# Performance work log

Measured on AMD Instinct MI355X. Metric: run time of the kernel, lower is better.

## Reference

```python
import jax, jax.numpy as jnp
import numpy as np

N = 100000   # graph nodes
E = 600000   # edges
D = 128      # feature_dim
K = 3        # candidate ops per MixedOp
EPS = 1e-5   # BatchNorm eps


def _param_stack(key, n_ops):
    kW, kb = jax.random.split(key)
    W = jax.random.normal(kW, (n_ops, K, D, D), jnp.float32) * (1.0 / np.sqrt(D))
    b = jax.random.normal(kb, (n_ops, K, D), jnp.float32) * 0.01
    g = jnp.ones((n_ops, K, D), jnp.float32)
    be = jnp.zeros((n_ops, K, D), jnp.float32)
    return W, b, g, be


def setup_inputs() -> dict:
    key = jax.random.key(0)
    ks = jax.random.split(key, 16)
    inp = {
        'src_emb': jax.random.normal(ks[0], (N, D), jnp.float32),
        'hr': jax.random.normal(ks[1], (N, D), jnp.float32),
        'edge_src': jax.random.randint(ks[2], (E,), 0, N),
        'edge_dst': jax.random.randint(ks[3], (E,), 0, N),
        'weights_zero': jax.random.uniform(ks[4], (1, K), jnp.float32),
        'weights_first': jax.random.uniform(ks[5], (3, K), jnp.float32),
        'weights_middle': jax.random.uniform(ks[6], (2, K), jnp.float32),
        'weights_last': jax.random.uniform(ks[7], (2, K), jnp.float32),
    }
    for name, k, n_ops in [('zero', ks[8], 1), ('first', ks[9], 3), ('mid', ks[10], 2), ('last', ks[11], 2)]:
        W, b, g, be = _param_stack(k, n_ops)
        inp[f'W_{name}'] = W; inp[f'b_{name}'] = b
        inp[f'g_{name}'] = g; inp[f'be_{name}'] = be
    inp['W_cat'] = jax.random.normal(ks[12], (3 * D, D), jnp.float32) * (1.0 / np.sqrt(3 * D))
    inp['b_cat'] = jax.random.normal(ks[13], (D,), jnp.float32) * 0.01
    inp['g_cat'] = jnp.ones((D,), jnp.float32)
    inp['be_cat'] = jnp.zeros((D,), jnp.float32)
    return inp


def _mean_agg(h, src, dst):
    s = jax.ops.segment_sum(h[src], dst, num_segments=N)            # [N,D]
    deg = jax.ops.segment_sum(jnp.ones((src.shape[0],), h.dtype), dst, num_segments=N)
    return s / jnp.maximum(deg, 1.0)[:, None]


def _max_agg(h, src, dst):
    m = jax.ops.segment_max(h[src], dst, num_segments=N)            # -inf for empty segs
    return jnp.where(jnp.isfinite(m), m, 0.0)


def _mixed(cands, w, W, b, g, be):
    # cands: list of K [N,D]; w:[K]; W:[K,D,D]; b/g/be:[K,D]
    x = jnp.stack(cands)                                            # [K,N,D]
    y = jnp.einsum('knd,kdf->knf', x, W) + b[:, None, :]            # Linear per candidate
    mu = jnp.mean(y, axis=1, keepdims=True)                         # BatchNorm1d (batch stats)
    var = jnp.var(y, axis=1, keepdims=True)
    y = (y - mu) * jax.lax.rsqrt(var + EPS) * g[:, None, :] + be[:, None, :]
    y = jax.nn.relu(y)
    return jnp.einsum('k,knd->nd', w, y)                            # alpha-weighted sum


def _graph_cands(h, src, dst):
    return [h, _mean_agg(h, src, dst), _max_agg(h, src, dst)]


def _cell_forward(src_emb, hr, edge_src, edge_dst,
                  weights_zero, weights_first, weights_middle, weights_last,
                  W_zero, b_zero, g_zero, be_zero,
                  W_first, b_first, g_first, be_first,
                  W_mid, b_mid, g_mid, be_mid,
                  W_last, b_last, g_last, be_last,
                  W_cat, b_cat, g_cat, be_cat):
    src, dst = edge_src, edge_dst
    # Cell_Zero: relation-composition candidates on (src_emb, hr)
    pre = [src_emb, src_emb - hr, src_emb * hr]
    h_in = _mixed(pre, weights_zero[0], W_zero[0], b_zero[0], g_zero[0], be_zero[0])
    # Cell_First (nodes=2): ops layout [(i=0,j=0),(i=1,j=0),(i=1,j=1)]
    states = [h_in]
    s0 = _mixed(_graph_cands(states[0], src, dst), weights_first[0], W_first[0], b_first[0], g_first[0], be_first[0])
    states.append(s0)
    s1 = (_mixed(_graph_cands(states[0], src, dst), weights_first[1], W_first[1], b_first[1], g_first[1], be_first[1])
          + _mixed(_graph_cands(states[1], src, dst), weights_first[2], W_first[2], b_first[2], g_first[2], be_first[2]))
    states.append(s1)
    states = states[1:]                                             # drop h_in -> len 2
    # Cell_Middle (nodes=2): one MixedOp per state
    states = [_mixed(_graph_cands(states[i], src, dst), weights_middle[i], W_mid[i], b_mid[i], g_mid[i], be_mid[i])
              for i in range(2)]
    # Cell_Last (in_nodes=2, nodes=1): one new state from both inputs; returns all 3
    s_last = (_mixed(_graph_cands(states[0], src, dst), weights_last[0], W_last[0], b_last[0], g_last[0], be_last[0])
              + _mixed(_graph_cands(states[1], src, dst), weights_last[1], W_last[1], b_last[1], g_last[1], be_last[1]))
    states = states + [s_last]                                      # len 3
    # concat -> Linear -> BN -> ReLU (dropout p=0)
    h = jnp.concatenate(states, axis=1) @ W_cat + b_cat             # [N,D]
    mu = jnp.mean(h, axis=0, keepdims=True)
    var = jnp.var(h, axis=0, keepdims=True)
    h = (h - mu) * jax.lax.rsqrt(var + EPS) * g_cat + be_cat
    return jax.nn.relu(h)


def reference(src_emb, hr, edge_src, edge_dst,
              weights_zero, weights_first, weights_middle, weights_last,
              W_zero, b_zero, g_zero, be_zero,
              W_first, b_first, g_first, be_first,
              W_mid, b_mid, g_mid, be_mid,
              W_last, b_last, g_last, be_last,
              W_cat, b_cat, g_cat, be_cat):
    return _cell_forward(src_emb, hr, edge_src, edge_dst,
                         weights_zero, weights_first, weights_middle, weights_last,
                         W_zero, b_zero, g_zero, be_zero,
                         W_first, b_first, g_first, be_first,
                         W_mid, b_mid, g_mid, be_mid,
                         W_last, b_last, g_last, be_last,
                         W_cat, b_cat, g_cat, be_cat)
```

## Files before the change

### kernel.cpp

```cpp
#include <hip/hip_runtime.h>

#define N_NODES 100000
#define N_EDGES 600000
#define NPAD    100096
#define NTILES  782
#define SCAN_B  98
#define EPS_F   1e-5f

typedef __bf16 bf16_t;
typedef __bf16 bf16x8 __attribute__((ext_vector_type(8)));
typedef __bf16 bf16x4 __attribute__((ext_vector_type(4)));
typedef float  f32x4  __attribute__((ext_vector_type(4)));

__global__ __launch_bounds__(256)
void init_zero_kernel(int* __restrict__ deg, float* __restrict__ stats)
{
    int i = blockIdx.x * 256 + threadIdx.x;
    if (i < N_NODES) deg[i] = 0;
    if (i < 9 * 768) stats[i] = 0.f;
}

__global__ __launch_bounds__(256)
void transpose_w_kernel(const float* __restrict__ Wz, const float* __restrict__ Wf,
                        const float* __restrict__ Wm, const float* __restrict__ Wl,
                        const float* __restrict__ Wc, bf16_t* __restrict__ wt)
{
    int idx = blockIdx.x * 256 + threadIdx.x;
    int mat = idx >> 14;
    int off = idx & 16383;
    int n = off >> 7, kk = off & 127;
    const float* src;
    if      (mat < 3)  src = Wz + mat * 16384;
    else if (mat < 12) src = Wf + (mat - 3) * 16384;
    else if (mat < 18) src = Wm + (mat - 12) * 16384;
    else if (mat < 24) src = Wl + (mat - 18) * 16384;
    else               src = Wc + (mat - 24) * 16384;
    wt[idx] = (bf16_t)src[kk * 128 + n];
}

__global__ __launch_bounds__(256)
void pre_kernel(const float* __restrict__ se, const float* __restrict__ hr,
                bf16_t* __restrict__ p0, bf16_t* __restrict__ p1, bf16_t* __restrict__ p2)
{
    long i = ((long)blockIdx.x * 256 + threadIdx.x) * 8;
    float4 a0 = *(const float4*)&se[i], a1 = *(const float4*)&se[i + 4];
    float4 b0 = *(const float4*)&hr[i], b1 = *(const float4*)&hr[i + 4];
    float av[8] = {a0.x, a0.y, a0.z, a0.w, a1.x, a1.y, a1.z, a1.w};
    float bv[8] = {b0.x, b0.y, b0.z, b0.w, b1.x, b1.y, b1.z, b1.w};
    bf16x8 o0, o1, o2;
#pragma unroll
    for (int j = 0; j < 8; ++j) {
        o0[j] = (bf16_t)av[j];
        o1[j] = (bf16_t)(av[j] - bv[j]);
        o2[j] = (bf16_t)(av[j] * bv[j]);
    }
    *(bf16x8*)&p0[i] = o0;
    *(bf16x8*)&p1[i] = o1;
    *(bf16x8*)&p2[i] = o2;
}

__global__ __launch_bounds__(256)
void deg_count_kernel(const int* __restrict__ dst, int* __restrict__ deg)
{
    int i = blockIdx.x * 256 + threadIdx.x;
    if (i < N_EDGES) atomicAdd(&deg[dst[i]], 1);
}

__global__ __launch_bounds__(256)
void scan_a_kernel(const int* __restrict__ deg, int* __restrict__ partials)
{
    __shared__ int ls[256];
    int b = blockIdx.x, t = threadIdx.x;
    int s = 0;
    for (int j = 0; j < 4; ++j) {
        int i = b * 1024 + t * 4 + j;
        if (i < N_NODES) s += deg[i];
    }
    ls[t] = s; __syncthreads();
    for (int o = 128; o > 0; o >>= 1) {
        if (t < o) ls[t] += ls[t + o];
        __syncthreads();
    }
    if (t == 0) partials[b] = ls[0];
}

__global__ void scan_b_kernel(const int* __restrict__ partials, int* __restrict__ pofs)
{
    if (threadIdx.x == 0) {
        int a = 0;
        for (int i = 0; i < SCAN_B; ++i) { pofs[i] = a; a += partials[i]; }
    }
}

__global__ __launch_bounds__(256)
void scan_c_kernel(const int* __restrict__ deg, const int* __restrict__ pofs,
                   int* __restrict__ row_ptr, int* __restrict__ cursor)
{
    __shared__ int ls[256];
    int b = blockIdx.x, t = threadIdx.x;
    int v[4], s = 0;
    for (int j = 0; j < 4; ++j) {
        int i = b * 1024 + t * 4 + j;
        v[j] = (i < N_NODES) ? deg[i] : 0;
        s += v[j];
    }
    ls[t] = s; __syncthreads();
    for (int o = 1; o < 256; o <<= 1) {
        int tv = (t >= o) ? ls[t - o] : 0;
        __syncthreads();
        ls[t] += tv;
        __syncthreads();
    }
    int excl = ls[t] - s + pofs[b];
    for (int j = 0; j < 4; ++j) {
        int i = b * 1024 + t * 4 + j;
        if (i < N_NODES) { row_ptr[i] = excl; cursor[i] = excl; excl += v[j]; }
    }
    if (b == 0 && t == 0) row_ptr[N_NODES] = N_EDGES;
}

__global__ __launch_bounds__(256)
void scatter_kernel(const int* __restrict__ src, const int* __restrict__ dst,
                    int* __restrict__ cursor, int* __restrict__ csr_src)
{
    int i = blockIdx.x * 256 + threadIdx.x;
    if (i < N_EDGES) {
        int p = atomicAdd(&cursor[dst[i]], 1);
        csr_src[p] = src[i];
    }
}

__global__ __launch_bounds__(256)
void agg_kernel(const bf16_t* __restrict__ h, const int* __restrict__ row_ptr,
                const int* __restrict__ csr_src,
                bf16_t* __restrict__ mean_o, bf16_t* __restrict__ max_o)
{
    int node = blockIdx.x * 16 + (threadIdx.x >> 4);
    int dd = (threadIdx.x & 15) * 8;
    int e0 = row_ptr[node], e1 = row_ptr[node + 1];
    float s[8], mx[8];
#pragma unroll
    for (int j = 0; j < 8; ++j) { s[j] = 0.f; mx[j] = 0.f; }
    for (int e = e0; e < e1; ++e) {
        int sc = csr_src[e];
        bf16x8 v = *(const bf16x8*)&h[(long)sc * 128 + dd];
#pragma unroll
        for (int j = 0; j < 8; ++j) {
            float f = (float)v[j];
            s[j] += f;
            mx[j] = fmaxf(mx[j], f);
        }
    }
    float inv = 1.f / fmaxf((float)(e1 - e0), 1.f);
    bf16x8 om, ox;
#pragma unroll
    for (int j = 0; j < 8; ++j) { om[j] = (bf16_t)(s[j] * inv); ox[j] = (bf16_t)mx[j]; }
    *(bf16x8*)&mean_o[(long)node * 128 + dd] = om;
    *(bf16x8*)&max_o [(long)node * 128 + dd] = ox;
}

__global__ __launch_bounds__(256, 2)
void gemm_kernel(const bf16_t* __restrict__ x0, const bf16_t* __restrict__ x1,
                 const bf16_t* __restrict__ x2, const bf16_t* __restrict__ wt,
                 const float* __restrict__ bias, bf16_t* __restrict__ out,
                 float* __restrict__ partial, int mode)
{
    __shared__ bf16_t lds_w[16384];
    __shared__ bf16_t lds_x[16384];
    const int tid  = threadIdx.x;
    const int lane = tid & 63;
    const int wave = tid >> 6;
    const int quad = lane >> 4;
    const int t16  = lane & 15;
    const int wr = wave >> 1, wc = wave & 1;
    const long tile_base = (long)blockIdx.x * 128;

    f32x4 acc[4][4];
#pragma unroll
    for (int a = 0; a < 4; ++a)
#pragma unroll
        for (int b = 0; b < 4; ++b) acc[a][b] = (f32x4){0.f, 0.f, 0.f, 0.f};

    const int k_sel = blockIdx.y;
    const int nchunk = (mode == 0) ? 1 : 3;
    const bf16_t* xk = (k_sel == 0) ? x0 : ((k_sel == 1) ? x1 : x2);
    bf16_t* outp = (mode == 0) ? (out + (long)k_sel * NPAD * 128) : out;
    const float* bp = (mode == 0) ? (bias + k_sel * 128) : bias;

    for (int c3 = 0; c3 < nchunk; ++c3) {
        const bf16_t* xcur = (mode == 0) ? xk : ((c3 == 0) ? x0 : ((c3 == 1) ? x1 : x2));
        const bf16_t* wcur = (mode == 0) ? (wt + k_sel * 16384) : (wt + c3 * 16384);
        if (c3) __syncthreads();
#pragma unroll
        for (int i = 0; i < 8; ++i) {
            int idx = tid + i * 256;
            int row = idx >> 4, c = idx & 15;
            int sw = c ^ (row & 15);
            *(uint4*)&lds_w[row * 128 + sw * 8] = *(const uint4*)&wcur[row * 128 + c * 8];
            *(uint4*)&lds_x[row * 128 + sw * 8] = *(const uint4*)&xcur[(tile_base + row) * 128 + c * 8];
        }
        __syncthreads();
#pragma unroll
        for (int ks = 0; ks < 4; ++ks) {
            bf16x8 xf[4], wf[4];
#pragma unroll
            for (int ms = 0; ms < 4; ++ms) {
                int row = wr * 64 + ms * 16 + t16;
                int sw = (ks * 4 + quad) ^ t16;
                xf[ms] = *(const bf16x8*)&lds_x[row * 128 + sw * 8];
            }
#pragma unroll
            for (int ns = 0; ns < 4; ++ns) {
                int row = wc * 64 + ns * 16 + t16;
                int sw = (ks * 4 + quad) ^ t16;
                wf[ns] = *(const bf16x8*)&lds_w[row * 128 + sw * 8];
            }
#pragma unroll
            for (int ns = 0; ns < 4; ++ns)
#pragma unroll
                for (int ms = 0; ms < 4; ++ms)
                    acc[ns][ms] = __builtin_amdgcn_mfma_f32_16x16x32_bf16(
                        wf[ns], xf[ms], acc[ns][ms], 0, 0, 0);
        }
    }

    float ss[16], sq[16];
#pragma unroll
    for (int i = 0; i < 16; ++i) { ss[i] = 0.f; sq[i] = 0.f; }

#pragma unroll
    for (int ms = 0; ms < 4; ++ms) {
        long m = tile_base + wr * 64 + ms * 16 + t16;
        if (m < N_NODES) {
#pragma unroll
            for (int ns = 0; ns < 4; ++ns) {
                int n0 = wc * 64 + ns * 16 + quad * 4;
                float4 b4 = *(const float4*)&bp[n0];
                float v0 = acc[ns][ms][0] + b4.x;
                float v1 = acc[ns][ms][1] + b4.y;
                float v2 = acc[ns][ms][2] + b4.z;
                float v3 = acc[ns][ms][3] + b4.w;
                ss[ns * 4 + 0] += v0; sq[ns * 4 + 0] += v0 * v0;
                ss[ns * 4 + 1] += v1; sq[ns * 4 + 1] += v1 * v1;
                ss[ns * 4 + 2] += v2; sq[ns * 4 + 2] += v2 * v2;
                ss[ns * 4 + 3] += v3; sq[ns * 4 + 3] += v3 * v3;
                bf16x4 ov;
                ov[0] = (bf16_t)v0; ov[1] = (bf16_t)v1;
                ov[2] = (bf16_t)v2; ov[3] = (bf16_t)v3;
                *(bf16x4*)&outp[m * 128 + n0] = ov;
            }
        }
    }

#pragma unroll
    for (int o = 1; o < 16; o <<= 1) {
#pragma unroll
        for (int i = 0; i < 16; ++i) {
            ss[i] += __shfl_xor(ss[i], o);
            sq[i] += __shfl_xor(sq[i], o);
        }
    }

    __syncthreads();
    float* lred = (float*)lds_w;
    if (t16 == 0) {
#pragma unroll
        for (int i = 0; i < 16; ++i) {
            lred[wave * 128 + quad * 32 + i]      = ss[i];
            lred[wave * 128 + quad * 32 + 16 + i] = sq[i];
        }
    }
    __syncthreads();
    {
        int t = tid;
        int d   = t & 127;
        int sel = (t >> 7) * 16;
        int dwc = d >> 6;
        int q   = (d >> 2) & 3;
        int i   = ((d >> 4) & 3) * 4 + (d & 3);
        float v = lred[(0 * 2 + dwc) * 128 + q * 32 + sel + i]
                + lred[(1 * 2 + dwc) * 128 + q * 32 + sel + i];
        long pidx = ((long)((mode == 0) ? k_sel : 0) * NTILES + blockIdx.x) * 256 + t;
        partial[pidx] = v;
    }
}

__global__ __launch_bounds__(256)
void reduce_stats_kernel(const float* __restrict__ partial, float* __restrict__ st)
{
    int k = blockIdx.x, j = blockIdx.y, t = threadIdx.x;
    int b0 = j * 98, b1 = (b0 + 98 < NTILES) ? b0 + 98 : NTILES;
    float s = 0.f;
    const float* p = partial + (long)k * NTILES * 256 + t;
    for (int b = b0; b < b1; ++b) s += p[(long)b * 256];
    atomicAdd(&st[k * 256 + t], s);
}

__global__ __launch_bounds__(256)
void passc_kernel(const bf16_t* __restrict__ y, const float* __restrict__ st,
                  const float* __restrict__ g, const float* __restrict__ be,
                  const float* __restrict__ w, bf16_t* __restrict__ out, int accflag)
{
    long base = ((long)blockIdx.x * 256 + threadIdx.x) * 8;
    int d0 = (int)(base & 127);
    const float invN = 1.0f / (float)N_NODES;
    float res[8];
    if (accflag) {
        bf16x8 pv = *(const bf16x8*)&out[base];
#pragma unroll
        for (int j = 0; j < 8; ++j) res[j] = (float)pv[j];
    } else {
#pragma unroll
        for (int j = 0; j < 8; ++j) res[j] = 0.f;
    }
#pragma unroll
    for (int k = 0; k < 3; ++k) {
        bf16x8 yv = *(const bf16x8*)&y[(long)k * NPAD * 128 + base];
        float wk = w[k];
#pragma unroll
        for (int j = 0; j < 8; ++j) {
            int d = d0 + j;
            float mu  = st[k * 256 + d] * invN;
            float var = st[k * 256 + 128 + d] * invN - mu * mu;
            float rs  = rsqrtf(var + EPS_F);
            float v = ((float)yv[j] - mu) * rs * g[k * 128 + d] + be[k * 128 + d];
            res[j] += wk * fmaxf(v, 0.f);
        }
    }
    bf16x8 ov;
#pragma unroll
    for (int j = 0; j < 8; ++j) ov[j] = (bf16_t)res[j];
    *(bf16x8*)&out[base] = ov;
}

__global__ __launch_bounds__(256)
void final_kernel(const bf16_t* __restrict__ h, const float* __restrict__ st,
                  const float* __restrict__ g, const float* __restrict__ be,
                  float* __restrict__ out)
{
    long base = ((long)blockIdx.x * 256 + threadIdx.x) * 8;
    int d0 = (int)(base & 127);
    const float invN = 1.0f / (float)N_NODES;
    bf16x8 hv = *(const bf16x8*)&h[base];
    float ov[8];
#pragma unroll
    for (int j = 0; j < 8; ++j) {
        int d = d0 + j;
        float mu  = st[d] * invN;
        float var = st[128 + d] * invN - mu * mu;
        float rs  = rsqrtf(var + EPS_F);
        float v = ((float)hv[j] - mu) * rs * g[d] + be[d];
        ov[j] = fmaxf(v, 0.f);
    }
    *(float4*)&out[base]     = (float4){ov[0], ov[1], ov[2], ov[3]};
    *(float4*)&out[base + 4] = (float4){ov[4], ov[5], ov[6], ov[7]};
}

extern "C" void kernel_launch(void* const* d_in, const int* in_sizes, int n_in,
                              void* d_out, int out_size, void* d_ws, size_t ws_size,
                              hipStream_t stream)
{
    const float* src_emb = (const float*)d_in[0];
    const float* hr      = (const float*)d_in[1];
    const int*   e_src   = (const int*)d_in[2];
    const int*   e_dst   = (const int*)d_in[3];
    const float* w_zero  = (const float*)d_in[4];
    const float* w_first = (const float*)d_in[5];
    const float* w_mid   = (const float*)d_in[6];
    const float* w_last  = (const float*)d_in[7];
    const float* W_zero  = (const float*)d_in[8];
    const float* b_zero  = (const float*)d_in[9];
    const float* g_zero  = (const float*)d_in[10];
    const float* be_zero = (const float*)d_in[11];
    const float* W_first = (const float*)d_in[12];
    const float* b_first = (const float*)d_in[13];
    const float* g_first = (const float*)d_in[14];
    const float* be_first= (const float*)d_in[15];
    const float* W_mid   = (const float*)d_in[16];
    const float* b_mid   = (const float*)d_in[17];
    const float* g_mid   = (const float*)d_in[18];
    const float* be_mid  = (const float*)d_in[19];
    const float* W_last  = (const float*)d_in[20];
    const float* b_last  = (const float*)d_in[21];
    const float* g_last  = (const float*)d_in[22];
    const float* be_last = (const float*)d_in[23];
    const float* W_cat   = (const float*)d_in[24];
    const float* b_cat   = (const float*)d_in[25];
    const float* g_cat   = (const float*)d_in[26];
    const float* be_cat  = (const float*)d_in[27];
    float* out = (float*)d_out;

    char* ws = (char*)d_ws;
    size_t off = 0;
    auto carve = [&](size_t bytes) -> char* {
        off = (off + 255) & ~(size_t)255;
        char* p = ws + off;
        off += bytes;
        return p;
    };

    const size_t SB = (size_t)NPAD * 128 * sizeof(bf16_t);
    bf16_t* B[8];
    for (int i = 0; i < 8; ++i) B[i] = (bf16_t*)carve(SB);
    bf16_t* ybuf = B[0];
    bf16_t* wt    = (bf16_t*)carve((size_t)27 * 16384 * 2);
    float*  stats = (float*)carve(9 * 768 * sizeof(float));
    float*  partial = (float*)carve((size_t)3 * NTILES * 256 * sizeof(float));
    int* deg    = (int*)carve((size_t)N_NODES * 4);
    int* rowp   = (int*)carve((size_t)(N_NODES + 1) * 4);
    int* cursor = (int*)carve((size_t)N_NODES * 4);
    int* csr    = (int*)carve((size_t)N_EDGES * 4);
    int* parts  = (int*)carve(SCAN_B * 4);
    int* pofs   = (int*)carve(SCAN_B * 4);

    bf16_t* wtZ  = wt;
    bf16_t* wtF0 = wt + (size_t)3  * 16384;
    bf16_t* wtF1 = wt + (size_t)6  * 16384;
    bf16_t* wtF2 = wt + (size_t)9  * 16384;
    bf16_t* wtM0 = wt + (size_t)12 * 16384;
    bf16_t* wtM1 = wt + (size_t)15 * 16384;
    bf16_t* wtL0 = wt + (size_t)18 * 16384;
    bf16_t* wtL1 = wt + (size_t)21 * 16384;
    bf16_t* wtC  = wt + (size_t)24 * 16384;

    float* st0 = stats + 0 * 768;
    float* st1 = stats + 1 * 768;
    float* st2 = stats + 2 * 768;
    float* st3 = stats + 3 * 768;
    float* st4 = stats + 4 * 768;
    float* st5 = stats + 5 * 768;
    float* st6 = stats + 6 * 768;
    float* st7 = stats + 7 * 768;
    float* st8 = stats + 8 * 768;

    const int GEL8 = (N_NODES * 128) / 2048;

    init_zero_kernel<<<dim3((N_NODES + 255) / 256), dim3(256), 0, stream>>>(deg, stats);
    transpose_w_kernel<<<dim3(1728), dim3(256), 0, stream>>>(W_zero, W_first, W_mid, W_last, W_cat, wt);
    deg_count_kernel<<<dim3((N_EDGES + 255) / 256), dim3(256), 0, stream>>>(e_dst, deg);
    scan_a_kernel<<<dim3(SCAN_B), dim3(256), 0, stream>>>(deg, parts);
    scan_b_kernel<<<dim3(1), dim3(64), 0, stream>>>(parts, pofs);
    scan_c_kernel<<<dim3(SCAN_B), dim3(256), 0, stream>>>(deg, pofs, rowp, cursor);
    scatter_kernel<<<dim3((N_EDGES + 255) / 256), dim3(256), 0, stream>>>(e_src, e_dst, cursor, csr);

    auto G = [&](const bf16_t* x0_, const bf16_t* x1_, const bf16_t* x2_,
                 const bf16_t* w_, const float* b_, bf16_t* o_, float* st_, int mode) {
        int nk = (mode == 0) ? 3 : 1;
        gemm_kernel<<<dim3(NTILES, nk), dim3(256), 0, stream>>>(
            x0_, x1_, x2_, w_, b_, o_, partial, mode);
        reduce_stats_kernel<<<dim3(nk, 8), dim3(256), 0, stream>>>(partial, st_);
    };
    auto C = [&](const float* g_, const float* be_, const float* w_, float* st_,
                 bf16_t* o_, int acc) {
        passc_kernel<<<dim3(GEL8), dim3(256), 0, stream>>>(ybuf, st_, g_, be_, w_, o_, acc);
    };
    auto A = [&](const bf16_t* h_, bf16_t* me_, bf16_t* mx_) {
        agg_kernel<<<dim3(N_NODES / 16), dim3(256), 0, stream>>>(h_, rowp, csr, me_, mx_);
    };

    pre_kernel<<<dim3(GEL8), dim3(256), 0, stream>>>(src_emb, hr, B[3], B[4], B[5]);
    G(B[3], B[4], B[5], wtZ, b_zero, ybuf, st0, 0);
    C(g_zero, be_zero, w_zero, st0, B[6], 0);

    A(B[6], B[3], B[4]);

    G(B[6], B[3], B[4], wtF0, b_first + 0 * 384, ybuf, st1, 0);
    C(g_first + 0 * 384, be_first + 0 * 384, w_first + 0, st1, B[5], 0);

    G(B[6], B[3], B[4], wtF1, b_first + 1 * 384, ybuf, st2, 0);
    C(g_first + 1 * 384, be_first + 1 * 384, w_first + 3, st2, B[7], 0);

    A(B[5], B[3], B[4]);

    G(B[5], B[3], B[4], wtF2, b_first + 2 * 384, ybuf, st3, 0);
    C(g_first + 2 * 384, be_first + 2 * 384, w_first + 6, st3, B[7], 1);

    G(B[5], B[3], B[4], wtM0, b_mid + 0 * 384, ybuf, st4, 0);
    C(g_mid + 0 * 384, be_mid + 0 * 384, w_mid + 0, st4, B[6], 0);

    A(B[7], B[3], B[4]);

    G(B[7], B[3], B[4], wtM1, b_mid + 1 * 384, ybuf, st5, 0);
    C(g_mid + 1 * 384, be_mid + 1 * 384, w_mid + 3, st5, B[5], 0);

    A(B[6], B[3], B[4]);
    G(B[6], B[3], B[4], wtL0, b_last + 0 * 384, ybuf, st6, 0);
    C(g_last + 0 * 384, be_last + 0 * 384, w_last + 0, st6, B[7], 0);
    A(B[5], B[3], B[4]);
    G(B[5], B[3], B[4], wtL1, b_last + 1 * 384, ybuf, st7, 0);
    C(g_last + 1 * 384, be_last + 1 * 384, w_last + 3, st7, B[7], 1);

    G(B[6], B[5], B[7], wtC, b_cat, B[0], st8, 1);
    final_kernel<<<dim3(GEL8), dim3(256), 0, stream>>>(B[0], st8, g_cat, be_cat, out);
}
```

Measured before the change: 1.247 ms.

## Load GEMM MFMA fragments directly from global memory, drop LDS staging

New measurement: 1.350 ms. 1.08x slower.

```diff
diff --git a/kernel.cpp b/kernel.cpp
--- a/kernel.cpp
+++ b/kernel.cpp
@@ -159,14 +159,13 @@
     *(bf16x8*)&max_o [(long)node * 128 + dd] = ox;
 }
 
-__global__ __launch_bounds__(256, 2)
+__global__ __launch_bounds__(256, 3)
 void gemm_kernel(const bf16_t* __restrict__ x0, const bf16_t* __restrict__ x1,
                  const bf16_t* __restrict__ x2, const bf16_t* __restrict__ wt,
                  const float* __restrict__ bias, bf16_t* __restrict__ out,
                  float* __restrict__ partial, int mode)
 {
-    __shared__ bf16_t lds_w[16384];
-    __shared__ bf16_t lds_x[16384];
+    __shared__ float lred[512];
     const int tid  = threadIdx.x;
     const int lane = tid & 63;
     const int wave = tid >> 6;
@@ -190,31 +189,18 @@
     for (int c3 = 0; c3 < nchunk; ++c3) {
         const bf16_t* xcur = (mode == 0) ? xk : ((c3 == 0) ? x0 : ((c3 == 1) ? x1 : x2));
         const bf16_t* wcur = (mode == 0) ? (wt + k_sel * 16384) : (wt + c3 * 16384);
-        if (c3) __syncthreads();
-#pragma unroll
-        for (int i = 0; i < 8; ++i) {
-            int idx = tid + i * 256;
-            int row = idx >> 4, c = idx & 15;
-            int sw = c ^ (row & 15);
-            *(uint4*)&lds_w[row * 128 + sw * 8] = *(const uint4*)&wcur[row * 128 + c * 8];
-            *(uint4*)&lds_x[row * 128 + sw * 8] = *(const uint4*)&xcur[(tile_base + row) * 128 + c * 8];
-        }
-        __syncthreads();
+        const bf16_t* wlane = wcur + (wc * 64 + t16) * 128 + quad * 8;
+        const bf16_t* xlane = xcur + (tile_base + wr * 64 + t16) * 128 + quad * 8;
 #pragma unroll
         for (int ks = 0; ks < 4; ++ks) {
-            bf16x8 xf[4], wf[4];
-#pragma unroll
-            for (int ms = 0; ms < 4; ++ms) {
-                int row = wr * 64 + ms * 16 + t16;
-                int sw = (ks * 4 + quad) ^ t16;
-                xf[ms] = *(const bf16x8*)&lds_x[row * 128 + sw * 8];
-            }
-#pragma unroll
-            for (int ns = 0; ns < 4; ++ns) {
-                int row = wc * 64 + ns * 16 + t16;
-                int sw = (ks * 4 + quad) ^ t16;
-                wf[ns] = *(const bf16x8*)&lds_w[row * 128 + sw * 8];
-            }
+            bf16x8 wf[4];
+#pragma unroll
+            for (int ns = 0; ns < 4; ++ns)
+                wf[ns] = *(const bf16x8*)&wlane[ns * 16 * 128 + ks * 32];
+            bf16x8 xf[4];
+#pragma unroll
+            for (int ms = 0; ms < 4; ++ms)
+                xf[ms] = *(const bf16x8*)&xlane[ms * 16 * 128 + ks * 32];
 #pragma unroll
             for (int ns = 0; ns < 4; ++ns)
 #pragma unroll
@@ -261,8 +247,6 @@
         }
     }
 
-    __syncthreads();
-    float* lred = (float*)lds_w;
     if (t16 == 0) {
 #pragma unroll
         for (int i = 0; i < 16; ++i) {
```

## Recompute GEMMs instead of storing pre-BN outputs; fuse BN-apply into second GEMM pass

Applied to the files above, without the earlier changes.

After: 1.270 ms. Within noise of the previous version (+1.8%).

```diff
diff --git a/kernel.cpp b/kernel.cpp
--- a/kernel.cpp
+++ b/kernel.cpp
@@ -160,10 +160,10 @@
 }
 
 __global__ __launch_bounds__(256, 2)
-void gemm_kernel(const bf16_t* __restrict__ x0, const bf16_t* __restrict__ x1,
-                 const bf16_t* __restrict__ x2, const bf16_t* __restrict__ wt,
-                 const float* __restrict__ bias, bf16_t* __restrict__ out,
-                 float* __restrict__ partial, int mode)
+void gemm_stats_kernel(const bf16_t* __restrict__ x0, const bf16_t* __restrict__ x1,
+                       const bf16_t* __restrict__ x2, const bf16_t* __restrict__ wt,
+                       const float* __restrict__ bias,
+                       float* __restrict__ partial, int mode)
 {
     __shared__ bf16_t lds_w[16384];
     __shared__ bf16_t lds_x[16384];
@@ -184,7 +184,6 @@
     const int k_sel = blockIdx.y;
     const int nchunk = (mode == 0) ? 1 : 3;
     const bf16_t* xk = (k_sel == 0) ? x0 : ((k_sel == 1) ? x1 : x2);
-    bf16_t* outp = (mode == 0) ? (out + (long)k_sel * NPAD * 128) : out;
     const float* bp = (mode == 0) ? (bias + k_sel * 128) : bias;
 
     for (int c3 = 0; c3 < nchunk; ++c3) {
@@ -244,10 +243,6 @@
                 ss[ns * 4 + 1] += v1; sq[ns * 4 + 1] += v1 * v1;
                 ss[ns * 4 + 2] += v2; sq[ns * 4 + 2] += v2 * v2;
                 ss[ns * 4 + 3] += v3; sq[ns * 4 + 3] += v3 * v3;
-                bf16x4 ov;
-                ov[0] = (bf16_t)v0; ov[1] = (bf16_t)v1;
-                ov[2] = (bf16_t)v2; ov[3] = (bf16_t)v3;
-                *(bf16x4*)&outp[m * 128 + n0] = ov;
             }
         }
     }
@@ -296,64 +291,191 @@
     atomicAdd(&st[k * 256 + t], s);
 }
 
-__global__ __launch_bounds__(256)
-void passc_kernel(const bf16_t* __restrict__ y, const float* __restrict__ st,
-                  const float* __restrict__ g, const float* __restrict__ be,
-                  const float* __restrict__ w, bf16_t* __restrict__ out, int accflag)
-{
-    long base = ((long)blockIdx.x * 256 + threadIdx.x) * 8;
-    int d0 = (int)(base & 127);
+__global__ __launch_bounds__(256, 2)
+void gemm_apply_kernel(const bf16_t* __restrict__ x0, const bf16_t* __restrict__ x1,
+                       const bf16_t* __restrict__ x2, const bf16_t* __restrict__ wt,
+                       const float* __restrict__ bias, const float* __restrict__ st,
+                       const float* __restrict__ g, const float* __restrict__ be,
+                       const float* __restrict__ wvec,
+                       bf16_t* __restrict__ outb, float* __restrict__ outf,
+                       int accflag, int mode)
+{
+    __shared__ bf16_t lds_w[16384];
+    __shared__ bf16_t lds_x[16384];
+    const int tid  = threadIdx.x;
+    const int lane = tid & 63;
+    const int wave = tid >> 6;
+    const int quad = lane >> 4;
+    const int t16  = lane & 15;
+    const int wr = wave >> 1, wc = wave & 1;
+    const long tile_base = (long)blockIdx.x * 128;
     const float invN = 1.0f / (float)N_NODES;
-    float res[8];
-    if (accflag) {
-        bf16x8 pv = *(const bf16x8*)&out[base];
-#pragma unroll
-        for (int j = 0; j < 8; ++j) res[j] = (float)pv[j];
+
+    f32x4 res[4][4];
+    if (mode == 0 && accflag) {
+#pragma unroll
+        for (int ms = 0; ms < 4; ++ms) {
+            long m = tile_base + wr * 64 + ms * 16 + t16;
+            bool ok = (m < N_NODES);
+#pragma unroll
+            for (int ns = 0; ns < 4; ++ns) {
+                int n0 = wc * 64 + ns * 16 + quad * 4;
+                if (ok) {
+                    bf16x4 pv = *(const bf16x4*)&outb[m * 128 + n0];
+                    res[ns][ms] = (f32x4){(float)pv[0], (float)pv[1], (float)pv[2], (float)pv[3]};
+                } else {
+                    res[ns][ms] = (f32x4){0.f, 0.f, 0.f, 0.f};
+                }
+            }
+        }
     } else {
 #pragma unroll
-        for (int j = 0; j < 8; ++j) res[j] = 0.f;
-    }
-#pragma unroll
+        for (int a = 0; a < 4; ++a)
+#pragma unroll
+            for (int b = 0; b < 4; ++b) res[a][b] = (f32x4){0.f, 0.f, 0.f, 0.f};
+    }
+
+    f32x4 acc[4][4];
+#pragma unroll
+    for (int a = 0; a < 4; ++a)
+#pragma unroll
+        for (int b = 0; b < 4; ++b) acc[a][b] = (f32x4){0.f, 0.f, 0.f, 0.f};
+
     for (int k = 0; k < 3; ++k) {
-        bf16x8 yv = *(const bf16x8*)&y[(long)k * NPAD * 128 + base];
-        float wk = w[k];
-#pragma unroll
-        for (int j = 0; j < 8; ++j) {
-            int d = d0 + j;
-            float mu  = st[k * 256 + d] * invN;
-            float var = st[k * 256 + 128 + d] * invN - mu * mu;
-            float rs  = rsqrtf(var + EPS_F);
-            float v = ((float)yv[j] - mu) * rs * g[k * 128 + d] + be[k * 128 + d];
-            res[j] += wk * fmaxf(v, 0.f);
-        }
-    }
-    bf16x8 ov;
-#pragma unroll
-    for (int j = 0; j < 8; ++j) ov[j] = (bf16_t)res[j];
-    *(bf16x8*)&out[base] = ov;
-}
-
-__global__ __launch_bounds__(256)
-void final_kernel(const bf16_t* __restrict__ h, const float* __restrict__ st,
-                  const float* __restrict__ g, const float* __restrict__ be,
-                  float* __restrict__ out)
-{
-    long base = ((long)blockIdx.x * 256 + threadIdx.x) * 8;
-    int d0 = (int)(base & 127);
-    const float invN = 1.0f / (float)N_NODES;
-    bf16x8 hv = *(const bf16x8*)&h[base];
-    float ov[8];
-#pragma unroll
-    for (int j = 0; j < 8; ++j) {
-        int d = d0 + j;
-        float mu  = st[d] * invN;
-        float var = st[128 + d] * invN - mu * mu;
-        float rs  = rsqrtf(var + EPS_F);
-        float v = ((float)hv[j] - mu) * rs * g[d] + be[d];
-        ov[j] = fmaxf(v, 0.f);
-    }
-    *(float4*)&out[base]     = (float4){ov[0], ov[1], ov[2], ov[3]};
-    *(float4*)&out[base + 4] = (float4){ov[4], ov[5], ov[6], ov[7]};
+        const bf16_t* xcur = (k == 0) ? x0 : ((k == 1) ? x1 : x2);
+        const bf16_t* wcur = wt + k * 16384;
+        if (k) __syncthreads();
+#pragma unroll
+        for (int i = 0; i < 8; ++i) {
+            int idx = tid + i * 256;
+            int row = idx >> 4, c = idx & 15;
+            int sw = c ^ (row & 15);
+            *(uint4*)&lds_w[row * 128 + sw * 8] = *(const uint4*)&wcur[row * 128 + c * 8];
+            *(uint4*)&lds_x[row * 128 + sw * 8] = *(const uint4*)&xcur[(tile_base + row) * 128 + c * 8];
+        }
+        __syncthreads();
+
+        if (mode == 0) {
+#pragma unroll
+            for (int a = 0; a < 4; ++a)
+#pragma unroll
+                for (int b = 0; b < 4; ++b) acc[a][b] = (f32x4){0.f, 0.f, 0.f, 0.f};
+        }
+
+#pragma unroll
+        for (int ks = 0; ks < 4; ++ks) {
+            bf16x8 xf[4], wf[4];
+#pragma unroll
+            for (int ms = 0; ms < 4; ++ms) {
+                int row = wr * 64 + ms * 16 + t16;
+                int sw = (ks * 4 + quad) ^ t16;
+                xf[ms] = *(const bf16x8*)&lds_x[row * 128 + sw * 8];
+            }
+#pragma unroll
+            for (int ns = 0; ns < 4; ++ns) {
+                int row = wc * 64 + ns * 16 + t16;
+                int sw = (ks * 4 + quad) ^ t16;
+                wf[ns] = *(const bf16x8*)&lds_w[row * 128 + sw * 8];
+            }
+#pragma unroll
+            for (int ns = 0; ns < 4; ++ns)
+#pragma unroll
+                for (int ms = 0; ms < 4; ++ms)
+                    acc[ns][ms] = __builtin_amdgcn_mfma_f32_16x16x32_bf16(
+                        wf[ns], xf[ms], acc[ns][ms], 0, 0, 0);
+        }
+
+        if (mode == 0) {
+            float wk = wvec[k];
+#pragma unroll
+            for (int ns = 0; ns < 4; ++ns) {
+                int n0 = wc * 64 + ns * 16 + quad * 4;
+                float4 sv = *(const float4*)&st[k * 256 + n0];
+                float4 qv = *(const float4*)&st[k * 256 + 128 + n0];
+                float4 gv = *(const float4*)&g[k * 128 + n0];
+                float4 ev = *(const float4*)&be[k * 128 + n0];
+                float4 bv = *(const float4*)&bias[k * 128 + n0];
+                float svx[4] = {sv.x, sv.y, sv.z, sv.w};
+                float qvx[4] = {qv.x, qv.y, qv.z, qv.w};
+                float gvx[4] = {gv.x, gv.y, gv.z, gv.w};
+                float evx[4] = {ev.x, ev.y, ev.z, ev.w};
+                float bvx[4] = {bv.x, bv.y, bv.z, bv.w};
+                f32x4 A, C;
+#pragma unroll
+                for (int j = 0; j < 4; ++j) {
+                    float mu  = svx[j] * invN;
+                    float var = qvx[j] * invN - mu * mu;
+                    float rs  = rsqrtf(var + EPS_F);
+                    A[j] = rs * gvx[j];
+                    C[j] = (bvx[j] - mu) * A[j] + evx[j];
+                }
+#pragma unroll
+                for (int ms = 0; ms < 4; ++ms)
+#pragma unroll
+                    for (int j = 0; j < 4; ++j)
+                        res[ns][ms][j] += wk * fmaxf(acc[ns][ms][j] * A[j] + C[j], 0.f);
+            }
+        }
+    }
+
+    if (mode == 0) {
+#pragma unroll
+        for (int ms = 0; ms < 4; ++ms) {
+            long m = tile_base + wr * 64 + ms * 16 + t16;
+            if (m < N_NODES) {
+#pragma unroll
+                for (int ns = 0; ns < 4; ++ns) {
+                    int n0 = wc * 64 + ns * 16 + quad * 4;
+                    bf16x4 ov;
+                    ov[0] = (bf16_t)res[ns][ms][0];
+                    ov[1] = (bf16_t)res[ns][ms][1];
+                    ov[2] = (bf16_t)res[ns][ms][2];
+                    ov[3] = (bf16_t)res[ns][ms][3];
+                    *(bf16x4*)&outb[m * 128 + n0] = ov;
+                }
+            }
+        }
+    } else {
+        f32x4 A4[4], C4[4];
+#pragma unroll
+        for (int ns = 0; ns < 4; ++ns) {
+            int n0 = wc * 64 + ns * 16 + quad * 4;
+            float4 sv = *(const float4*)&st[n0];
+            float4 qv = *(const float4*)&st[128 + n0];
+            float4 gv = *(const float4*)&g[n0];
+            float4 ev = *(const float4*)&be[n0];
+            float4 bv = *(const float4*)&bias[n0];
+            float svx[4] = {sv.x, sv.y, sv.z, sv.w};
+            float qvx[4] = {qv.x, qv.y, qv.z, qv.w};
+            float gvx[4] = {gv.x, gv.y, gv.z, gv.w};
+            float evx[4] = {ev.x, ev.y, ev.z, ev.w};
+            float bvx[4] = {bv.x, bv.y, bv.z, bv.w};
+#pragma unroll
+            for (int j = 0; j < 4; ++j) {
+                float mu  = svx[j] * invN;
+                float var = qvx[j] * invN - mu * mu;
+                float rs  = rsqrtf(var + EPS_F);
+                A4[ns][j] = rs * gvx[j];
+                C4[ns][j] = (bvx[j] - mu) * A4[ns][j] + evx[j];
+            }
+        }
+#pragma unroll
+        for (int ms = 0; ms < 4; ++ms) {
+            long m = tile_base + wr * 64 + ms * 16 + t16;
+            if (m < N_NODES) {
+#pragma unroll
+                for (int ns = 0; ns < 4; ++ns) {
+                    int n0 = wc * 64 + ns * 16 + quad * 4;
+                    float4 o;
+                    o.x = fmaxf(acc[ns][ms][0] * A4[ns][0] + C4[ns][0], 0.f);
+                    o.y = fmaxf(acc[ns][ms][1] * A4[ns][1] + C4[ns][1], 0.f);
+                    o.z = fmaxf(acc[ns][ms][2] * A4[ns][2] + C4[ns][2], 0.f);
+                    o.w = fmaxf(acc[ns][ms][3] * A4[ns][3] + C4[ns][3], 0.f);
+                    *(float4*)&outf[m * 128 + n0] = o;
+                }
+            }
+        }
+    }
 }
 
 extern "C" void kernel_launch(void* const* d_in, const int* in_sizes, int n_in,
@@ -400,9 +522,8 @@
     };
 
     const size_t SB = (size_t)NPAD * 128 * sizeof(bf16_t);
-    bf16_t* B[8];
-    for (int i = 0; i < 8; ++i) B[i] = (bf16_t*)carve(SB);
-    bf16_t* ybuf = B[0];
+    bf16_t* B[6];
+    for (int i = 0; i < 6; ++i) B[i] = (bf16_t*)carve(SB);
     bf16_t* wt    = (bf16_t*)carve((size_t)27 * 16384 * 2);
     float*  stats = (float*)carve(9 * 768 * sizeof(float));
     float*  partial = (float*)carve((size_t)3 * NTILES * 256 * sizeof(float));
@@ -443,53 +564,65 @@
     scan_c_kernel<<<dim3(SCAN_B), dim3(256), 0, stream>>>(deg, pofs, rowp, cursor);
     scatter_kernel<<<dim3((N_EDGES + 255) / 256), dim3(256), 0, stream>>>(e_src, e_dst, cursor, csr);
 
-    auto G = [&](const bf16_t* x0_, const bf16_t* x1_, const bf16_t* x2_,
-                 const bf16_t* w_, const float* b_, bf16_t* o_, float* st_, int mode) {
+    auto S = [&](const bf16_t* x0_, const bf16_t* x1_, const bf16_t* x2_,
+                 const bf16_t* w_, const float* b_, float* st_, int mode) {
         int nk = (mode == 0) ? 3 : 1;
-        gemm_kernel<<<dim3(NTILES, nk), dim3(256), 0, stream>>>(
-            x0_, x1_, x2_, w_, b_, o_, partial, mode);
+        gemm_stats_kernel<<<dim3(NTILES, nk), dim3(256), 0, stream>>>(
+            x0_, x1_, x2_, w_, b_, partial, mode);
         reduce_stats_kernel<<<dim3(nk, 8), dim3(256), 0, stream>>>(partial, st_);
     };
-    auto C = [&](const float* g_, const float* be_, const float* w_, float* st_,
+    auto P = [&](const bf16_t* x0_, const bf16_t* x1_, const bf16_t* x2_,
+                 const bf16_t* w_, const float* b_, float* st_,
+                 const float* g_, const float* be_, const float* wv_,
                  bf16_t* o_, int acc) {
-        passc_kernel<<<dim3(GEL8), dim3(256), 0, stream>>>(ybuf, st_, g_, be_, w_, o_, acc);
+        gemm_apply_kernel<<<dim3(NTILES), dim3(256), 0, stream>>>(
+            x0_, x1_, x2_, w_, b_, st_, g_, be_, wv_, o_, nullptr, acc, 0);
     };
     auto A = [&](const bf16_t* h_, bf16_t* me_, bf16_t* mx_) {
         agg_kernel<<<dim3(N_NODES / 16), dim3(256), 0, stream>>>(h_, rowp, csr, me_, mx_);
     };
 
-    pre_kernel<<<dim3(GEL8), dim3(256), 0, stream>>>(src_emb, hr, B[3], B[4], B[5]);
-    G(B[3], B[4], B[5], wtZ, b_zero, ybuf, st0, 0);
-    C(g_zero, be_zero, w_zero, st0, B[6], 0);
-
-    A(B[6], B[3], B[4]);
-
-    G(B[6], B[3], B[4], wtF0, b_first + 0 * 384, ybuf, st1, 0);
-    C(g_first + 0 * 384, be_first + 0 * 384, w_first + 0, st1, B[5], 0);
-
-    G(B[6], B[3], B[4], wtF1, b_first + 1 * 384, ybuf, st2, 0);
-    C(g_first + 1 * 384, be_first + 1 * 384, w_first + 3, st2, B[7], 0);
-
-    A(B[5], B[3], B[4]);
-
-    G(B[5], B[3], B[4], wtF2, b_first + 2 * 384, ybuf, st3, 0);
-    C(g_first + 2 * 384, be_first + 2 * 384, w_first + 6, st3, B[7], 1);
-
-    G(B[5], B[3], B[4], wtM0, b_mid + 0 * 384, ybuf, st4, 0);
-    C(g_mid + 0 * 384, be_mid + 0 * 384, w_mid + 0, st4, B[6], 0);
-
-    A(B[7], B[3], B[4]);
-
-    G(B[7], B[3], B[4], wtM1, b_mid + 1 * 384, ybuf, st5, 0);
-    C(g_mid + 1 * 384, be_mid + 1 * 384, w_mid + 3, st5, B[5], 0);
-
-    A(B[6], B[3], B[4]);
-    G(B[6], B[3], B[4], wtL0, b_last + 0 * 384, ybuf, st6, 0);
-    C(g_last + 0 * 384, be_last + 0 * 384, w_last + 0, st6, B[7], 0);
-    A(B[5], B[3], B[4]);
-    G(B[5], B[3], B[4], wtL1, b_last + 1 * 384, ybuf, st7, 0);
-    C(g_last + 1 * 384, be_last + 1 * 384, w_last + 3, st7, B[7], 1);
-
-    G(B[6], B[5], B[7], wtC, b_cat, B[0], st8, 1);
-    final_kernel<<<dim3(GEL8), dim3(256), 0, stream>>>(B[0], st8, g_cat, be_cat, out);
-}
+    pre_kernel<<<dim3(GEL8), dim3(256), 0, stream>>>(src_emb, hr, B[0], B[1], B[2]);
+    S(B[0], B[1], B[2], wtZ, b_zero, st0, 0);
+    P(B[0], B[1], B[2], wtZ, b_zero, st0, g_zero, be_zero, w_zero, B[3], 0);
+
+    A(B[3], B[4], B[5]);
+
+    S(B[3], B[4], B[5], wtF0, b_first + 0 * 384, st1, 0);
+    P(B[3], B[4], B[5], wtF0, b_first + 0 * 384, st1,
+      g_first + 0 * 384, be_first + 0 * 384, w_first + 0, B[0], 0);
+
+    S(B[3], B[4], B[5], wtF1, b_first + 1 * 384, st2, 0);
+    P(B[3], B[4], B[5], wtF1, b_first + 1 * 384, st2,
+      g_first + 1 * 384, be_first + 1 * 384, w_first + 3, B[1], 0);
+
+    A(B[0], B[2], B[3]);
+
+    S(B[0], B[2], B[3], wtF2, b_first + 2 * 384, st3, 0);
+    P(B[0], B[2], B[3], wtF2, b_first + 2 * 384, st3,
+      g_first + 2 * 384, be_first + 2 * 384, w_first + 6, B[1], 1);
+
+    S(B[0], B[2], B[3], wtM0, b_mid + 0 * 384, st4, 0);
+    P(B[0], B[2], B[3], wtM0, b_mid + 0 * 384, st4,
+      g_mid + 0 * 384, be_mid + 0 * 384, w_mid + 0, B[4], 0);
+
+    A(B[1], B[0], B[2]);
+
+    S(B[1], B[0], B[2], wtM1, b_mid + 1 * 384, st5, 0);
+    P(B[1], B[0], B[2], wtM1, b_mid + 1 * 384, st5,
+      g_mid + 1 * 384, be_mid + 1 * 384, w_mid + 3, B[5], 0);
+
+    A(B[4], B[0], B[1]);
+    S(B[4], B[0], B[1], wtL0, b_last + 0 * 384, st6, 0);
+    P(B[4], B[0], B[1], wtL0, b_last + 0 * 384, st6,
+      g_last + 0 * 384, be_last + 0 * 384, w_last + 0, B[2], 0);
+    A(B[5], B[0], B[1]);
+    S(B[5], B[0], B[1], wtL1, b_last + 1 * 384, st7, 0);
+    P(B[5], B[0], B[1], wtL1, b_last + 1 * 384, st7,
+      g_last + 1 * 384, be_last + 1 * 384, w_last + 3, B[2], 1);
+
+    S(B[4], B[5], B[2], wtC, b_cat, st8, 1);
+    gemm_apply_kernel<<<dim3(NTILES), dim3(256), 0, stream>>>(
+        B[4], B[5], B[2], wtC, b_cat, st8, g_cat, be_cat, w_zero,
+        nullptr, out, 0, 1);
+}
```
